# Performance work log

Hardware: AMD Instinct MI355X
Metric: run time of the kernel (lower is better)

## Reference

```python
import jax, jax.numpy as jnp
import numpy as np

B, L = 256, 32768

def _avg_pool1d(x, k, p):
    # count_include_pad=True avg pool via prefix sums: O(L) instead of O(L*k)
    xp = jnp.pad(x, ((0, 0), (0, 0), (p, p)))
    cs = jnp.cumsum(xp, axis=-1)
    cs = jnp.pad(cs, ((0, 0), (0, 0), (1, 0)))  # leading zero for window diff
    return (cs[..., k:] - cs[..., :-k]) / k

def setup_inputs() -> dict:
    key = jax.random.key(0)
    x = jax.random.normal(key, (B, L), dtype=jnp.float32)
    return {"x": x}

def reference(x):
    x = x[:, None, :]  # [B, 1, L]
    # log(max(1, 1+x)) and log(max(1, 1-x)): cat-with-ones + max == clamp at 1
    a = jnp.log(jnp.maximum(1.0, 1.0 + x))
    b = jnp.log(jnp.maximum(1.0, 1.0 - x))
    a0 = _avg_pool1d(a, 3, 1)
    a5 = _avg_pool1d(a, 199, 99)
    b0 = _avg_pool1d(b, 3, 1)
    b5 = _avg_pool1d(b, 199, 99)
    return jnp.concatenate([a0 - a5, a0, b0 - b5, b0], axis=1)  # [B, 4, L]
```

## Files before the change

### kernel.cpp

```cpp
#include <hip/hip_runtime.h>

#define B_DIM 256
#define L_DIM 32768
#define CHUNK 2048
#define HALO  100
#define NTOT  (CHUNK + 2*HALO)
#define NG    (NTOT/4)
#define T     256
#define EPT   9

typedef float fx4 __attribute__((ext_vector_type(4)));

__global__ __launch_bounds__(T) void pool_feat_kernel(const float* __restrict__ x,
                                                      float* __restrict__ out) {
    const int row    = blockIdx.y;
    const int chunk0 = blockIdx.x * CHUNK;
    const int tid    = threadIdx.x;

    __shared__ __align__(16) float sA[NTOT];
    __shared__ __align__(16) float sB[NTOT];
    __shared__ float waveA[4];
    __shared__ float waveB[4];

    const float* xr = x + (size_t)row * L_DIM;

    for (int g = tid; g < NG; g += T) {
        const int c = chunk0 - HALO + 4 * g;
        fx4 v;
        if (c >= 0 && c + 3 < L_DIM) {
            v = *reinterpret_cast<const fx4*>(xr + c);
        } else {
            v.x = (c + 0 >= 0 && c + 0 < L_DIM) ? xr[c + 0] : 0.0f;
            v.y = (c + 1 >= 0 && c + 1 < L_DIM) ? xr[c + 1] : 0.0f;
            v.z = (c + 2 >= 0 && c + 2 < L_DIM) ? xr[c + 2] : 0.0f;
            v.w = (c + 3 >= 0 && c + 3 < L_DIM) ? xr[c + 3] : 0.0f;
        }
        *reinterpret_cast<fx4*>(&sA[4 * g]) = v;
    }
    __syncthreads();

    const int s0 = tid * EPT;
    const int s1 = min(NTOT, s0 + EPT);
    float ra[EPT], rb[EPT];
    float runA = 0.0f, runB = 0.0f;
    #pragma unroll
    for (int j = 0; j < EPT; ++j) {
        const int idx = s0 + j;
        const float v = (idx < s1) ? sA[idx] : 0.0f;
        const float t = __logf(1.0f + fabsf(v));
        runA += (v > 0.0f) ? t : 0.0f;
        runB += (v < 0.0f) ? t : 0.0f;
        ra[j] = runA; rb[j] = runB;
    }

    float vA = runA, vB = runB;
    const int lane = tid & 63;
    const int wid  = tid >> 6;
    #pragma unroll
    for (int d = 1; d < 64; d <<= 1) {
        float uA = __shfl_up(vA, d);
        float uB = __shfl_up(vB, d);
        if (lane >= d) { vA += uA; vB += uB; }
    }
    if (lane == 63) { waveA[wid] = vA; waveB[wid] = vB; }
    __syncthreads();
    float offA = vA - runA;
    float offB = vB - runB;
    #pragma unroll
    for (int w = 0; w < 3; ++w) {
        if (w < wid) { offA += waveA[w]; offB += waveB[w]; }
    }

    #pragma unroll
    for (int j = 0; j < EPT; ++j) {
        const int idx = s0 + j;
        if (idx < NTOT) { sA[idx] = ra[j] + offA; sB[idx] = rb[j] + offB; }
    }
    __syncthreads();

    const float inv3   = 1.0f / 3.0f;
    const float inv199 = 1.0f / 199.0f;
    float* ob = out + (size_t)row * 4u * L_DIM + chunk0;
    #pragma unroll
    for (int it = 0; it < CHUNK / (4 * T); ++it) {
        const int i0 = 4 * (tid + it * T);
        fx4 r0, r1, r2, r3;
        #pragma unroll
        for (int arr = 0; arr < 2; ++arr) {
            const float* s = arr ? sB : sA;
            const fx4 L0 = *reinterpret_cast<const fx4*>(s + i0);
            const fx4 L1 = *reinterpret_cast<const fx4*>(s + i0 + 96);
            const fx4 L2 = *reinterpret_cast<const fx4*>(s + i0 + 100);
            const fx4 L3 = *reinterpret_cast<const fx4*>(s + i0 + 104);
            const fx4 L4 = *reinterpret_cast<const fx4*>(s + i0 + 196);
            const fx4 L5 = *reinterpret_cast<const fx4*>(s + i0 + 200);
            const float csI[4]   = {L0.x, L0.y, L0.z, L0.w};
            const float cs98[4]  = {L1.z, L1.w, L2.x, L2.y};
            const float cs101[4] = {L2.y, L2.z, L2.w, L3.x};
            const float cs199[4] = {L4.w, L5.x, L5.y, L5.z};
            fx4& rs = arr ? r3 : r1;
            fx4& rd = arr ? r2 : r0;
            #pragma unroll
            for (int u = 0; u < 4; ++u) {
                const float p0 = (cs101[u] - cs98[u]) * inv3;
                const float p5 = (cs199[u] - csI[u]) * inv199;
                rs[u] = p0;
                rd[u] = p0 - p5;
            }
        }
        *reinterpret_cast<fx4*>(ob + 0 * (size_t)L_DIM + i0) = r0;
        *reinterpret_cast<fx4*>(ob + 1 * (size_t)L_DIM + i0) = r1;
        *reinterpret_cast<fx4*>(ob + 2 * (size_t)L_DIM + i0) = r2;
        *reinterpret_cast<fx4*>(ob + 3 * (size_t)L_DIM + i0) = r3;
    }
}

extern "C" void kernel_launch(void* const* d_in, const int* in_sizes, int n_in,
                              void* d_out, int out_size, void* d_ws, size_t ws_size,
                              hipStream_t stream) {
    const float* x = (const float*)d_in[0];
    float* out = (float*)d_out;
    dim3 grid(L_DIM / CHUNK, B_DIM);
    pool_feat_kernel<<<grid, dim3(T), 0, stream>>>(x, out);
}
```

Measured before the change: 32.61 us.

## Process two chunks per block with register-prefetched input for the next chunk

Each block now handles two consecutive chunks of a row. The next chunk's input is loaded into registers while the current chunk is scanned and pooled, which is meant to hide global load latency. The scan stores the signed log value in shared memory and does a second pass instead of holding per-element register arrays, which lowers register pressure. The grid is halved, so there is less parallelism, and an extra barrier and shared-memory pass are added per chunk.

```diff
diff --git a/kernel.cpp b/kernel.cpp
--- a/kernel.cpp
+++ b/kernel.cpp
@@ -8,14 +8,35 @@
 #define NG    (NTOT/4)
 #define T     256
 #define EPT   9
+#define NCH   2
+#define NR    3
 
 typedef float fx4 __attribute__((ext_vector_type(4)));
 
+__device__ __forceinline__ void issue_loads(const float* __restrict__ xr, int chunk0,
+                                            int tid, fx4 p[NR]) {
+    #pragma unroll
+    for (int r = 0; r < NR; ++r) {
+        const int g = tid + r * T;
+        if (g < NG) {
+            const int c = chunk0 - HALO + 4 * g;
+            if (c >= 0 && c + 3 < L_DIM) {
+                p[r] = *reinterpret_cast<const fx4*>(xr + c);
+            } else {
+                p[r].x = (c + 0 >= 0 && c + 0 < L_DIM) ? xr[c + 0] : 0.0f;
+                p[r].y = (c + 1 >= 0 && c + 1 < L_DIM) ? xr[c + 1] : 0.0f;
+                p[r].z = (c + 2 >= 0 && c + 2 < L_DIM) ? xr[c + 2] : 0.0f;
+                p[r].w = (c + 3 >= 0 && c + 3 < L_DIM) ? xr[c + 3] : 0.0f;
+            }
+        }
+    }
+}
+
 __global__ __launch_bounds__(T) void pool_feat_kernel(const float* __restrict__ x,
                                                       float* __restrict__ out) {
-    const int row    = blockIdx.y;
-    const int chunk0 = blockIdx.x * CHUNK;
-    const int tid    = threadIdx.x;
+    const int row  = blockIdx.y;
+    const int base = blockIdx.x * (CHUNK * NCH);
+    const int tid  = threadIdx.x;
 
     __shared__ __align__(16) float sA[NTOT];
     __shared__ __align__(16) float sB[NTOT];
@@ -24,94 +45,101 @@
 
     const float* xr = x + (size_t)row * L_DIM;
 
-    for (int g = tid; g < NG; g += T) {
-        const int c = chunk0 - HALO + 4 * g;
-        fx4 v;
-        if (c >= 0 && c + 3 < L_DIM) {
-            v = *reinterpret_cast<const fx4*>(xr + c);
-        } else {
-            v.x = (c + 0 >= 0 && c + 0 < L_DIM) ? xr[c + 0] : 0.0f;
-            v.y = (c + 1 >= 0 && c + 1 < L_DIM) ? xr[c + 1] : 0.0f;
-            v.z = (c + 2 >= 0 && c + 2 < L_DIM) ? xr[c + 2] : 0.0f;
-            v.w = (c + 3 >= 0 && c + 3 < L_DIM) ? xr[c + 3] : 0.0f;
+    fx4 pc[NR], pn[NR];
+    issue_loads(xr, base, tid, pc);
+
+    for (int k = 0; k < NCH; ++k) {
+        const int chunk0 = base + k * CHUNK;
+
+        #pragma unroll
+        for (int r = 0; r < NR; ++r) {
+            const int g = tid + r * T;
+            if (g < NG) *reinterpret_cast<fx4*>(&sA[4 * g]) = pc[r];
         }
-        *reinterpret_cast<fx4*>(&sA[4 * g]) = v;
-    }
-    __syncthreads();
+        if (k + 1 < NCH) issue_loads(xr, chunk0 + CHUNK, tid, pn);
+        __syncthreads();
 
-    const int s0 = tid * EPT;
-    const int s1 = min(NTOT, s0 + EPT);
-    float ra[EPT], rb[EPT];
-    float runA = 0.0f, runB = 0.0f;
-    #pragma unroll
-    for (int j = 0; j < EPT; ++j) {
-        const int idx = s0 + j;
-        const float v = (idx < s1) ? sA[idx] : 0.0f;
-        const float t = __logf(1.0f + fabsf(v));
-        runA += (v > 0.0f) ? t : 0.0f;
-        runB += (v < 0.0f) ? t : 0.0f;
-        ra[j] = runA; rb[j] = runB;
-    }
+        const int s0 = tid * EPT;
+        const int s1 = min(NTOT, s0 + EPT);
+        float runA = 0.0f, runB = 0.0f;
+        for (int j = s0; j < s1; ++j) {
+            const float v = sA[j];
+            const float t = __logf(1.0f + fabsf(v));
+            const float u = copysignf(t, v);
+            runA += fmaxf(u, 0.0f);
+            runB += fmaxf(-u, 0.0f);
+            sA[j] = u;
+        }
 
-    float vA = runA, vB = runB;
-    const int lane = tid & 63;
-    const int wid  = tid >> 6;
-    #pragma unroll
-    for (int d = 1; d < 64; d <<= 1) {
-        float uA = __shfl_up(vA, d);
-        float uB = __shfl_up(vB, d);
-        if (lane >= d) { vA += uA; vB += uB; }
-    }
-    if (lane == 63) { waveA[wid] = vA; waveB[wid] = vB; }
-    __syncthreads();
-    float offA = vA - runA;
-    float offB = vB - runB;
-    #pragma unroll
-    for (int w = 0; w < 3; ++w) {
-        if (w < wid) { offA += waveA[w]; offB += waveB[w]; }
-    }
+        float vA = runA, vB = runB;
+        const int lane = tid & 63;
+        const int wid  = tid >> 6;
+        #pragma unroll
+        for (int d = 1; d < 64; d <<= 1) {
+            float uA = __shfl_up(vA, d);
+            float uB = __shfl_up(vB, d);
+            if (lane >= d) { vA += uA; vB += uB; }
+        }
+        if (lane == 63) { waveA[wid] = vA; waveB[wid] = vB; }
+        __syncthreads();
+        float offA = vA - runA;
+        float offB = vB - runB;
+        #pragma unroll
+        for (int w = 0; w < 3; ++w) {
+            if (w < wid) { offA += waveA[w]; offB += waveB[w]; }
+        }
 
-    #pragma unroll
-    for (int j = 0; j < EPT; ++j) {
-        const int idx = s0 + j;
-        if (idx < NTOT) { sA[idx] = ra[j] + offA; sB[idx] = rb[j] + offB; }
-    }
-    __syncthreads();
+        float accA = offA, accB = offB;
+        for (int j = s0; j < s1; ++j) {
+            const float u = sA[j];
+            accA += fmaxf(u, 0.0f);
+            accB += fmaxf(-u, 0.0f);
+            sA[j] = accA;
+            sB[j] = accB;
+        }
+        __syncthreads();
 
-    const float inv3   = 1.0f / 3.0f;
-    const float inv199 = 1.0f / 199.0f;
-    float* ob = out + (size_t)row * 4u * L_DIM + chunk0;
-    #pragma unroll
-    for (int it = 0; it < CHUNK / (4 * T); ++it) {
-        const int i0 = 4 * (tid + it * T);
-        fx4 r0, r1, r2, r3;
+        const float inv3   = 1.0f / 3.0f;
+        const float inv199 = 1.0f / 199.0f;
+        float* ob = out + (size_t)row * 4u * L_DIM + chunk0;
         #pragma unroll
-        for (int arr = 0; arr < 2; ++arr) {
-            const float* s = arr ? sB : sA;
-            const fx4 L0 = *reinterpret_cast<const fx4*>(s + i0);
-            const fx4 L1 = *reinterpret_cast<const fx4*>(s + i0 + 96);
-            const fx4 L2 = *reinterpret_cast<const fx4*>(s + i0 + 100);
-            const fx4 L3 = *reinterpret_cast<const fx4*>(s + i0 + 104);
-            const fx4 L4 = *reinterpret_cast<const fx4*>(s + i0 + 196);
-            const fx4 L5 = *reinterpret_cast<const fx4*>(s + i0 + 200);
-            const float csI[4]   = {L0.x, L0.y, L0.z, L0.w};
-            const float cs98[4]  = {L1.z, L1.w, L2.x, L2.y};
-            const float cs101[4] = {L2.y, L2.z, L2.w, L3.x};
-            const float cs199[4] = {L4.w, L5.x, L5.y, L5.z};
-            fx4& rs = arr ? r3 : r1;
-            fx4& rd = arr ? r2 : r0;
+        for (int it = 0; it < CHUNK / (4 * T); ++it) {
+            const int i0 = 4 * (tid + it * T);
+            fx4 r0, r1, r2, r3;
             #pragma unroll
-            for (int u = 0; u < 4; ++u) {
-                const float p0 = (cs101[u] - cs98[u]) * inv3;
-                const float p5 = (cs199[u] - csI[u]) * inv199;
-                rs[u] = p0;
-                rd[u] = p0 - p5;
+            for (int arr = 0; arr < 2; ++arr) {
+                const float* s = arr ? sB : sA;
+                const fx4 L0 = *reinterpret_cast<const fx4*>(s + i0);
+                const fx4 L1 = *reinterpret_cast<const fx4*>(s + i0 + 96);
+                const fx4 L2 = *reinterpret_cast<const fx4*>(s + i0 + 100);
+                const fx4 L3 = *reinterpret_cast<const fx4*>(s + i0 + 104);
+                const fx4 L4 = *reinterpret_cast<const fx4*>(s + i0 + 196);
+                const fx4 L5 = *reinterpret_cast<const fx4*>(s + i0 + 200);
+                const float csI[4]   = {L0.x, L0.y, L0.z, L0.w};
+                const float cs98[4]  = {L1.z, L1.w, L2.x, L2.y};
+                const float cs101[4] = {L2.y, L2.z, L2.w, L3.x};
+                const float cs199[4] = {L4.w, L5.x, L5.y, L5.z};
+                fx4& rs = arr ? r3 : r1;
+                fx4& rd = arr ? r2 : r0;
+                #pragma unroll
+                for (int u = 0; u < 4; ++u) {
+                    const float p0 = (cs101[u] - cs98[u]) * inv3;
+                    const float p5 = (cs199[u] - csI[u]) * inv199;
+                    rs[u] = p0;
+                    rd[u] = p0 - p5;
+                }
             }
+            *reinterpret_cast<fx4*>(ob + 0 * (size_t)L_DIM + i0) = r0;
+            *reinterpret_cast<fx4*>(ob + 1 * (size_t)L_DIM + i0) = r1;
+            *reinterpret_cast<fx4*>(ob + 2 * (size_t)L_DIM + i0) = r2;
+            *reinterpret_cast<fx4*>(ob + 3 * (size_t)L_DIM + i0) = r3;
         }
-        *reinterpret_cast<fx4*>(ob + 0 * (size_t)L_DIM + i0) = r0;
-        *reinterpret_cast<fx4*>(ob + 1 * (size_t)L_DIM + i0) = r1;
-        *reinterpret_cast<fx4*>(ob + 2 * (size_t)L_DIM + i0) = r2;
-        *reinterpret_cast<fx4*>(ob + 3 * (size_t)L_DIM + i0) = r3;
+
+        if (k + 1 < NCH) {
+            __syncthreads();
+            #pragma unroll
+            for (int r = 0; r < NR; ++r) pc[r] = pn[r];
+        }
     }
 }
 
@@ -120,6 +148,6 @@
                               hipStream_t stream) {
     const float* x = (const float*)d_in[0];
     float* out = (float*)d_out;
-    dim3 grid(L_DIM / CHUNK, B_DIM);
+    dim3 grid(L_DIM / (CHUNK * NCH), B_DIM);
     pool_feat_kernel<<<grid, dim3(T), 0, stream>>>(x, out);
 }
```

New measurement: 31.10 us. 1.05x faster.
